# Optimization experiments

Hardware: AMD Instinct MI355X
Metric: run time of the kernel (lower is better)

The kernel has to match this reference:

```python
import jax, jax.numpy as jnp
import numpy as np

B = 8192       # batch (tokens)
D = 2048       # data_dim
DEPTH = 3      # tree depth: 1 root + 2 mid + 4 leaf experts
INIT = 0.02


def setup_inputs() -> dict:
    key = jax.random.key(0)
    ks = jax.random.split(key, 6)
    x = jax.random.normal(ks[0], (B, D), dtype=jnp.float32)
    # router output simulated as i.i.d. path bits (router is a frozen pretrained black box)
    path_mask = jax.random.randint(ks[1], (B, DEPTH), 0, 2, dtype=jnp.int32)
    W0 = jax.random.normal(ks[2], (D, D), dtype=jnp.float32) * INIT
    b0 = jnp.zeros((D,), dtype=jnp.float32)
    W1 = jax.random.normal(ks[3], (2, D, D), dtype=jnp.float32) * INIT  # depth-1 experts
    b1 = jnp.zeros((2, D), dtype=jnp.float32)
    W2 = jax.random.normal(ks[4], (4, D, D), dtype=jnp.float32) * INIT  # depth-2 (leaf) experts
    b2 = jnp.zeros((4, D), dtype=jnp.float32)
    return {"x": x, "W0": W0, "b0": b0, "W1": W1, "b1": b1,
            "W2": W2, "b2": b2, "path_mask": path_mask}


def reference(x, W0, b0, W1, b1, W2, b2, path_mask):
    # Root expert (depth 0): applied to all tokens.
    h0 = jax.nn.relu(x @ W0 + b0)                                  # [B, D]
    bit0 = path_mask[:, 0]                                          # routes depth-1 children
    bit1 = path_mask[:, 1]                                          # routes depth-2 children
    # Depth-1: 2 experts; dense compute then per-token select (static-shape MoE dispatch).
    h1_all = jax.nn.relu(jnp.einsum('bd,edf->bef', h0, W1) + b1)    # [B, 2, D]
    h1 = jnp.take_along_axis(h1_all, bit0[:, None, None].astype(jnp.int32), axis=1)[:, 0]
    # Depth-2 (leaves): 4 experts indexed by the 2-bit path.
    leaf = 2 * bit0 + bit1                                          # [B] in {0,1,2,3}
    h2_all = jax.nn.relu(jnp.einsum('bd,edf->bef', h1, W2) + b2)    # [B, 4, D]
    y = jnp.take_along_axis(h2_all, leaf[:, None, None].astype(jnp.int32), axis=1)[:, 0]
    return y
```

## Files before the change

kernel.cpp:

```cpp
#include <hip/hip_runtime.h>

#define BB 8192
#define DD 2048
#define NSLOT 7
#define NP1 (BB + 2*128)
#define NP2 (BB + 4*128)

typedef unsigned short u16;
typedef unsigned int   u32;
typedef unsigned long long u64;

typedef __bf16 bf16x8 __attribute__((ext_vector_type(8)));
typedef float  f32x4  __attribute__((ext_vector_type(4)));
typedef u16    u16x8  __attribute__((ext_vector_type(8)));

#define OFF_WT   0ull
#define OFF_XB   (OFF_WT + (size_t)NSLOT*DD*DD*2)
#define OFF_H0   (OFF_XB + (size_t)BB*DD*2)
#define OFF_P1   (OFF_H0 + (size_t)BB*DD*2)
#define OFF_P2   (OFF_P1 + (size_t)NP1*4)
#define OFF_META (OFF_P2 + (size_t)NP2*4)

__device__ __forceinline__ u16 f2bf(float f) {
  u32 u = __float_as_uint(f);
  u32 r = (u + 0x7FFFu + ((u >> 16) & 1u)) >> 16;
  return (u16)r;
}
__device__ __forceinline__ float bf2f(u16 u) {
  return __uint_as_float(((u32)u) << 16);
}

__device__ __forceinline__ void gld16(const void* g, void* l) {
  __builtin_amdgcn_global_load_lds(
      (const __attribute__((address_space(1))) void*)g,
      (__attribute__((address_space(3))) void*)l, 16, 0, 0);
}


__global__ void k_detect(const u16* x, int* meta) {
  __shared__ int cnt, cntz;
  if (threadIdx.x == 0) { cnt = 0; cntz = 0; }
  __syncthreads();
  u16 u = x[threadIdx.x * 17];
  int ex = (u >> 7) & 0xFF;
  int sane = (ex == 0) || (ex >= 112 && ex <= 143);
  atomicAdd(&cnt, sane);
  atomicAdd(&cntz, (u == 0) ? 1 : 0);
  __syncthreads();
  if (threadIdx.x == 0) meta[20] = (cnt >= 205 && cntz < 64) ? 1 : 0;
}

__global__ __launch_bounds__(1024) void k_route(const int* __restrict__ pm,
                                                int* __restrict__ p1,
                                                int* __restrict__ p2,
                                                int* __restrict__ meta) {
  __shared__ int cnt[6];
  __shared__ int cur[6];
  __shared__ int base1[2], base2[4];
  const int tid = threadIdx.x;
  const int lane = tid & 63;
  if (tid < 6) { cnt[tid] = 0; cur[tid] = 0; }
  __syncthreads();

  for (int i = tid; i < NP1; i += 1024) p1[i] = -1;
  for (int i = tid; i < NP2; i += 1024) p2[i] = -1;

  int myb0[8], myleaf[8];
  #pragma unroll
  for (int i = 0; i < 8; ++i) {
    int b = i * 1024 + tid;
    int b0 = pm[b*3] & 1, b1 = pm[b*3+1] & 1;
    myb0[i] = b0; myleaf[i] = b0*2 + b1;
  }
  #pragma unroll
  for (int i = 0; i < 8; ++i) {
    u64 m0 = __ballot(myb0[i] == 0);
    if (lane == 0) {
      atomicAdd(&cnt[0], __popcll(m0));
      atomicAdd(&cnt[1], 64 - __popcll(m0));
    }
    #pragma unroll
    for (int e = 0; e < 4; ++e) {
      u64 me = __ballot(myleaf[i] == e);
      if (lane == 0) atomicAdd(&cnt[2+e], __popcll(me));
    }
  }
  __syncthreads();
  if (tid == 0) {
    base1[0] = 0;
    base1[1] = (cnt[0] + 127) & ~127;
    meta[12] = 0; meta[13] = base1[1];
    meta[14] = base1[1] + ((cnt[1] + 127) & ~127);
    int b = 0;
    #pragma unroll
    for (int e = 0; e < 4; ++e) {
      base2[e] = b; meta[15+e] = b;
      b += (cnt[2+e] + 127) & ~127;
    }
    meta[19] = b;
  }
  __syncthreads();
  #pragma unroll
  for (int i = 0; i < 8; ++i) {
    int b = i * 1024 + tid;
    u64 lt = (1ull << lane) - 1ull;
    #pragma unroll
    for (int g = 0; g < 2; ++g) {
      u64 m = __ballot(myb0[i] == g);
      int pos = __popcll(m & lt);
      int wbase = 0;
      if (lane == 0 && m) wbase = atomicAdd(&cur[g], __popcll(m));
      wbase = __shfl(wbase, 0);
      if (myb0[i] == g) p1[base1[g] + wbase + pos] = b;
    }
    #pragma unroll
    for (int g = 0; g < 4; ++g) {
      u64 m = __ballot(myleaf[i] == g);
      int pos = __popcll(m & lt);
      int wbase = 0;
      if (lane == 0 && m) wbase = atomicAdd(&cur[2+g], __popcll(m));
      wbase = __shfl(wbase, 0);
      if (myleaf[i] == g) p2[base2[g] + wbase + pos] = b;
    }
  }
}

__global__ void k_cvtx(const void* __restrict__ x, u16* __restrict__ xb,
                       const int* __restrict__ meta) {
  int i = blockIdx.x * 256 + threadIdx.x;
  if (meta[20]) {
    ((uint4*)xb)[i] = ((const uint4*)x)[i];
  } else {
    const float4* p = (const float4*)x + (size_t)i * 2;
    float4 a = p[0], b = p[1];
    uint4 o;
    o.x = f2bf(a.x) | ((u32)f2bf(a.y) << 16);
    o.y = f2bf(a.z) | ((u32)f2bf(a.w) << 16);
    o.z = f2bf(b.x) | ((u32)f2bf(b.y) << 16);
    o.w = f2bf(b.z) | ((u32)f2bf(b.w) << 16);
    ((uint4*)xb)[i] = o;
  }
}

__global__ void k_wt(const void* __restrict__ W0, const void* __restrict__ W1,
                     const void* __restrict__ W2, u16* __restrict__ wt,
                     const int* __restrict__ meta) {
  __shared__ u16 tile[64][66];
  int bid = blockIdx.x;
  int slot = bid >> 10;
  int t = bid & 1023;
  int tr = t >> 5, tc = t & 31;
  const void* src; size_t eoff;
  if (slot == 0)      { src = W0; eoff = 0; }
  else if (slot <= 2) { src = W1; eoff = (size_t)(slot-1)*DD*DD; }
  else                { src = W2; eoff = (size_t)(slot-3)*DD*DD; }
  int r0 = tr*64, c0 = tc*64;
  int tid = threadIdx.x;
  int isbf = meta[20];
  #pragma unroll
  for (int i = 0; i < 4; ++i) {
    int idx = tid + i*256;
    int r = idx >> 4, c4 = (idx & 15) * 4;
    size_t goff = eoff + (size_t)(r0 + r)*DD + c0 + c4;
    u16 v0, v1, v2, v3;
    if (isbf) {
      ushort4 v = *(const ushort4*)((const u16*)src + goff);
      v0 = v.x; v1 = v.y; v2 = v.z; v3 = v.w;
    } else {
      float4 v = *(const float4*)((const float*)src + goff);
      v0 = f2bf(v.x); v1 = f2bf(v.y); v2 = f2bf(v.z); v3 = f2bf(v.w);
    }
    tile[r][c4+0] = v0; tile[r][c4+1] = v1;
    tile[r][c4+2] = v2; tile[r][c4+3] = v3;
  }
  __syncthreads();
  u16* dst = wt + (size_t)slot*DD*DD;
  #pragma unroll
  for (int i = 0; i < 2; ++i) {
    int idx = tid + i*256;
    int n = idx >> 3, j = idx & 7;
    u16x8 o;
    #pragma unroll
    for (int k = 0; k < 8; ++k) o[k] = tile[j*8 + k][n];
    *(u16x8*)&dst[(size_t)(c0 + n)*DD + r0 + j*8] = o;
  }
}

__global__ __launch_bounds__(256, 2) void k_gemm(
    const u16* __restrict__ A, const u16* __restrict__ Wt,
    const void* __restrict__ bias, const int* __restrict__ perm,
    const int* __restrict__ bases, int nexp,
    void* __restrict__ Out, int final_out, const int* __restrict__ meta) {
  __shared__ __align__(16) u16 As[128*32];
  __shared__ __align__(16) u16 Bs[128*32];

  const int tid  = threadIdx.x;
  const int wid  = tid >> 6;
  const int lane = tid & 63;
  const int m0 = blockIdx.y * 128;
  const int n0 = blockIdx.x * 128;

  int e = 0;
  if (nexp == 2)      e = (m0 >= bases[1]);
  else if (nexp == 4) e = (m0 >= bases[1]) + (m0 >= bases[2]) + (m0 >= bases[3]);
  const u16* W = Wt + (size_t)e * DD * DD;

  const u16* gA[2]; const u16* gB[2];
  u16* lA[2]; u16* lB[2];
  #pragma unroll
  for (int p = 0; p < 2; ++p) {
    int seg   = p*4 + wid;
    int boff  = seg*1024 + lane*16;
    int row   = boff >> 6;
    int chunk = (boff >> 4) & 3;
    int kk    = (chunk ^ ((row >> 1) & 3)) * 8;
    int gr = m0 + row;
    if (perm) { int t = perm[gr]; gr = (t < 0) ? 0 : t; }
    gA[p] = A + (size_t)gr * DD + kk;
    gB[p] = W + (size_t)(n0 + row) * DD + kk;
    lA[p] = (u16*)((char*)As + seg*1024);
    lB[p] = (u16*)((char*)Bs + seg*1024);
  }

  f32x4 zero = {0.0f, 0.0f, 0.0f, 0.0f};
  f32x4 acc[4][4];
  #pragma unroll
  for (int i = 0; i < 4; ++i)
    #pragma unroll
    for (int j = 0; j < 4; ++j) acc[i][j] = zero;

  const int wm = wid & 1, wn = wid >> 1;
  const int q = lane >> 4, cl = lane & 15;
  const int sw = q ^ ((cl >> 1) & 3);
  const int aoff  = (wm*64 + cl) * 32 + sw*8;
  const int boff2 = (wn*64 + cl) * 32 + sw*8;

  for (int k0 = 0; k0 < DD; k0 += 32) {
    gld16(gA[0] + k0, lA[0]);
    gld16(gA[1] + k0, lA[1]);
    gld16(gB[0] + k0, lB[0]);
    gld16(gB[1] + k0, lB[1]);
    __syncthreads();
    bf16x8 af[4], bf[4];
    #pragma unroll
    for (int mt = 0; mt < 4; ++mt) af[mt] = *(const bf16x8*)&As[aoff + mt*16*32];
    #pragma unroll
    for (int nt = 0; nt < 4; ++nt) bf[nt] = *(const bf16x8*)&Bs[boff2 + nt*16*32];
    #pragma unroll
    for (int mt = 0; mt < 4; ++mt)
      #pragma unroll
      for (int nt = 0; nt < 4; ++nt)
        acc[mt][nt] = __builtin_amdgcn_mfma_f32_16x16x32_bf16(af[mt], bf[nt], acc[mt][nt], 0, 0, 0);
    __syncthreads();
  }

  const int isbf = meta[20];
  float bv[4];
  #pragma unroll
  for (int nt = 0; nt < 4; ++nt) {
    int col = n0 + wn*64 + nt*16 + cl;
    bv[nt] = isbf ? bf2f(((const u16*)bias)[e*DD + col])
                  : ((const float*)bias)[e*DD + col];
  }
  #pragma unroll
  for (int mt = 0; mt < 4; ++mt) {
    int rbase = m0 + wm*64 + mt*16 + q*4;
    #pragma unroll
    for (int r = 0; r < 4; ++r) {
      int row = rbase + r;
      int orow = row;
      if (perm) { orow = perm[row]; if (orow < 0) continue; }
      #pragma unroll
      for (int nt = 0; nt < 4; ++nt) {
        int col = n0 + wn*64 + nt*16 + cl;
        float v = acc[mt][nt][r] + bv[nt];
        v = v > 0.0f ? v : 0.0f;
        if (!final_out || isbf) ((u16*)Out)[(size_t)orow*DD + col] = f2bf(v);
        else                    ((float*)Out)[(size_t)orow*DD + col] = v;
      }
    }
  }
}

extern "C" void kernel_launch(void* const* d_in, const int* in_sizes, int n_in,
                              void* d_out, int out_size, void* d_ws, size_t ws_size,
                              hipStream_t stream) {
  (void)in_sizes; (void)n_in; (void)out_size; (void)ws_size;
  const void* x  = d_in[0];
  const void* W0 = d_in[1];
  const void* b0 = d_in[2];
  const void* W1 = d_in[3];
  const void* b1 = d_in[4];
  const void* W2 = d_in[5];
  const void* b2 = d_in[6];
  const int*  pm = (const int*)d_in[7];

  char* ws  = (char*)d_ws;
  u16*  wt  = (u16*)(ws + OFF_WT);
  u16*  xb  = (u16*)(ws + OFF_XB);
  u16*  h0  = (u16*)(ws + OFF_H0);
  u16*  h1  = xb;
  int*  p1  = (int*)(ws + OFF_P1);
  int*  p2  = (int*)(ws + OFF_P2);
  int*  meta= (int*)(ws + OFF_META);

  hipLaunchKernelGGL(k_detect, dim3(1),  dim3(256),  0, stream, (const u16*)x, meta);
  hipLaunchKernelGGL(k_route,  dim3(1),  dim3(1024), 0, stream, pm, p1, p2, meta);
  hipLaunchKernelGGL(k_cvtx,   dim3(BB*DD/8/256), dim3(256), 0, stream, x, xb, meta);
  hipLaunchKernelGGL(k_wt,     dim3(7*1024), dim3(256), 0, stream, W0, W1, W2, wt, meta);

  hipLaunchKernelGGL(k_gemm, dim3(16, 64), dim3(256), 0, stream,
                     xb, wt, b0, (const int*)nullptr, (const int*)nullptr, 1,
                     (void*)h0, 0, meta);
  hipLaunchKernelGGL(k_gemm, dim3(16, 66), dim3(256), 0, stream,
                     h0, wt + (size_t)1*DD*DD, b1, p1, meta + 12, 2,
                     (void*)h1, 0, meta);
  hipLaunchKernelGGL(k_gemm, dim3(16, 68), dim3(256), 0, stream,
                     h1, wt + (size_t)3*DD*DD, b2, p2, meta + 15, 4,
                     d_out, 1, meta);
}
```

Measured before the change: 540.8 us.

## Fuse setup kernels into one launch and double-buffer GEMM LDS tiles

Merges the dtype-detect, routing, x conversion and weight transpose kernels into a single k_setup launch. Each block now recomputes the bf16 detection with a wavefront ballot instead of reading it from a prior kernel, which removes three launches and their serialization. The GEMM main loop moves to a two-buffer LDS scheme: the next K-slice is prefetched while MFMAs run on the current one, with one barrier per iteration instead of two. This doubles the GEMM's LDS use and relies on every block reaching the same detection result independently.

```diff
diff --git a/kernel.cpp b/kernel.cpp
--- a/kernel.cpp
+++ b/kernel.cpp
@@ -36,153 +36,147 @@
       (__attribute__((address_space(3))) void*)l, 16, 0, 0);
 }
 
-
-__global__ void k_detect(const u16* x, int* meta) {
-  __shared__ int cnt, cntz;
-  if (threadIdx.x == 0) { cnt = 0; cntz = 0; }
-  __syncthreads();
-  u16 u = x[threadIdx.x * 17];
+__device__ __forceinline__ int detect_bf(const u16* x) {
+  int lane = threadIdx.x & 63;
+  u16 u = x[lane * 33];
   int ex = (u >> 7) & 0xFF;
   int sane = (ex == 0) || (ex >= 112 && ex <= 143);
-  atomicAdd(&cnt, sane);
-  atomicAdd(&cntz, (u == 0) ? 1 : 0);
-  __syncthreads();
-  if (threadIdx.x == 0) meta[20] = (cnt >= 205 && cntz < 64) ? 1 : 0;
-}
-
-__global__ __launch_bounds__(1024) void k_route(const int* __restrict__ pm,
-                                                int* __restrict__ p1,
-                                                int* __restrict__ p2,
-                                                int* __restrict__ meta) {
-  __shared__ int cnt[6];
-  __shared__ int cur[6];
-  __shared__ int base1[2], base2[4];
+  u64 ms = __ballot(sane != 0);
+  u64 mz = __ballot(u == 0);
+  return (__popcll(ms) >= 52) && (__popcll(mz) < 16);
+}
+
+__global__ __launch_bounds__(256) void k_setup(
+    const void* __restrict__ xv, const void* __restrict__ W0,
+    const void* __restrict__ W1, const void* __restrict__ W2,
+    const int* __restrict__ pm, u16* __restrict__ xb, u16* __restrict__ wt,
+    int* __restrict__ p1, int* __restrict__ p2, int* __restrict__ meta) {
+  const int bid = blockIdx.x;
   const int tid = threadIdx.x;
-  const int lane = tid & 63;
-  if (tid < 6) { cnt[tid] = 0; cur[tid] = 0; }
-  __syncthreads();
-
-  for (int i = tid; i < NP1; i += 1024) p1[i] = -1;
-  for (int i = tid; i < NP2; i += 1024) p2[i] = -1;
-
-  int myb0[8], myleaf[8];
-  #pragma unroll
-  for (int i = 0; i < 8; ++i) {
-    int b = i * 1024 + tid;
-    int b0 = pm[b*3] & 1, b1 = pm[b*3+1] & 1;
-    myb0[i] = b0; myleaf[i] = b0*2 + b1;
-  }
-  #pragma unroll
-  for (int i = 0; i < 8; ++i) {
-    u64 m0 = __ballot(myb0[i] == 0);
-    if (lane == 0) {
-      atomicAdd(&cnt[0], __popcll(m0));
-      atomicAdd(&cnt[1], 64 - __popcll(m0));
-    }
-    #pragma unroll
-    for (int e = 0; e < 4; ++e) {
-      u64 me = __ballot(myleaf[i] == e);
-      if (lane == 0) atomicAdd(&cnt[2+e], __popcll(me));
-    }
-  }
-  __syncthreads();
-  if (tid == 0) {
-    base1[0] = 0;
-    base1[1] = (cnt[0] + 127) & ~127;
-    meta[12] = 0; meta[13] = base1[1];
-    meta[14] = base1[1] + ((cnt[1] + 127) & ~127);
-    int b = 0;
-    #pragma unroll
-    for (int e = 0; e < 4; ++e) {
-      base2[e] = b; meta[15+e] = b;
-      b += (cnt[2+e] + 127) & ~127;
-    }
-    meta[19] = b;
-  }
-  __syncthreads();
-  #pragma unroll
-  for (int i = 0; i < 8; ++i) {
-    int b = i * 1024 + tid;
-    u64 lt = (1ull << lane) - 1ull;
-    #pragma unroll
-    for (int g = 0; g < 2; ++g) {
-      u64 m = __ballot(myb0[i] == g);
-      int pos = __popcll(m & lt);
-      int wbase = 0;
-      if (lane == 0 && m) wbase = atomicAdd(&cur[g], __popcll(m));
-      wbase = __shfl(wbase, 0);
-      if (myb0[i] == g) p1[base1[g] + wbase + pos] = b;
-    }
-    #pragma unroll
-    for (int g = 0; g < 4; ++g) {
-      u64 m = __ballot(myleaf[i] == g);
-      int pos = __popcll(m & lt);
-      int wbase = 0;
-      if (lane == 0 && m) wbase = atomicAdd(&cur[2+g], __popcll(m));
-      wbase = __shfl(wbase, 0);
-      if (myleaf[i] == g) p2[base2[g] + wbase + pos] = b;
-    }
-  }
-}
-
-__global__ void k_cvtx(const void* __restrict__ x, u16* __restrict__ xb,
-                       const int* __restrict__ meta) {
-  int i = blockIdx.x * 256 + threadIdx.x;
-  if (meta[20]) {
-    ((uint4*)xb)[i] = ((const uint4*)x)[i];
-  } else {
-    const float4* p = (const float4*)x + (size_t)i * 2;
-    float4 a = p[0], b = p[1];
-    uint4 o;
-    o.x = f2bf(a.x) | ((u32)f2bf(a.y) << 16);
-    o.y = f2bf(a.z) | ((u32)f2bf(a.w) << 16);
-    o.z = f2bf(b.x) | ((u32)f2bf(b.y) << 16);
-    o.w = f2bf(b.z) | ((u32)f2bf(b.w) << 16);
-    ((uint4*)xb)[i] = o;
-  }
-}
-
-__global__ void k_wt(const void* __restrict__ W0, const void* __restrict__ W1,
-                     const void* __restrict__ W2, u16* __restrict__ wt,
-                     const int* __restrict__ meta) {
-  __shared__ u16 tile[64][66];
-  int bid = blockIdx.x;
-  int slot = bid >> 10;
-  int t = bid & 1023;
-  int tr = t >> 5, tc = t & 31;
-  const void* src; size_t eoff;
-  if (slot == 0)      { src = W0; eoff = 0; }
-  else if (slot <= 2) { src = W1; eoff = (size_t)(slot-1)*DD*DD; }
-  else                { src = W2; eoff = (size_t)(slot-3)*DD*DD; }
-  int r0 = tr*64, c0 = tc*64;
-  int tid = threadIdx.x;
-  int isbf = meta[20];
-  #pragma unroll
-  for (int i = 0; i < 4; ++i) {
-    int idx = tid + i*256;
-    int r = idx >> 4, c4 = (idx & 15) * 4;
-    size_t goff = eoff + (size_t)(r0 + r)*DD + c0 + c4;
-    u16 v0, v1, v2, v3;
+  const u16* x = (const u16*)xv;
+
+  if (bid == 0) {
+    int isbf = detect_bf(x);
+    if (tid == 0) meta[20] = isbf;
+    __shared__ int cnt[6], cur[6], base1[2], base2[4];
+    const int lane = tid & 63;
+    if (tid < 6) { cnt[tid] = 0; cur[tid] = 0; }
+    __syncthreads();
+    for (int i = tid; i < NP1; i += 256) p1[i] = -1;
+    for (int i = tid; i < NP2; i += 256) p2[i] = -1;
+    for (int c = 0; c < 32; ++c) {
+      int b = c * 256 + tid;
+      int b0 = pm[b*3] & 1, b1v = pm[b*3+1] & 1;
+      int leaf = b0*2 + b1v;
+      u64 m0 = __ballot(b0 == 0);
+      if (lane == 0) {
+        atomicAdd(&cnt[0], __popcll(m0));
+        atomicAdd(&cnt[1], 64 - __popcll(m0));
+      }
+      #pragma unroll
+      for (int e = 0; e < 4; ++e) {
+        u64 me = __ballot(leaf == e);
+        if (lane == 0) atomicAdd(&cnt[2+e], __popcll(me));
+      }
+    }
+    __syncthreads();
+    if (tid == 0) {
+      base1[0] = 0;
+      base1[1] = (cnt[0] + 127) & ~127;
+      meta[12] = 0; meta[13] = base1[1];
+      meta[14] = base1[1] + ((cnt[1] + 127) & ~127);
+      int b = 0;
+      #pragma unroll
+      for (int e = 0; e < 4; ++e) {
+        base2[e] = b; meta[15+e] = b;
+        b += (cnt[2+e] + 127) & ~127;
+      }
+    }
+    __syncthreads();
+    for (int c = 0; c < 32; ++c) {
+      int b = c * 256 + tid;
+      int b0 = pm[b*3] & 1, b1v = pm[b*3+1] & 1;
+      int leaf = b0*2 + b1v;
+      u64 lt = (1ull << lane) - 1ull;
+      #pragma unroll
+      for (int g = 0; g < 2; ++g) {
+        u64 m = __ballot(b0 == g);
+        int pos = __popcll(m & lt);
+        int wbase = 0;
+        if (lane == 0 && m) wbase = atomicAdd(&cur[g], __popcll(m));
+        wbase = __shfl(wbase, 0);
+        if (b0 == g) p1[base1[g] + wbase + pos] = b;
+      }
+      #pragma unroll
+      for (int g = 0; g < 4; ++g) {
+        u64 m = __ballot(leaf == g);
+        int pos = __popcll(m & lt);
+        int wbase = 0;
+        if (lane == 0 && m) wbase = atomicAdd(&cur[2+g], __popcll(m));
+        wbase = __shfl(wbase, 0);
+        if (leaf == g) p2[base2[g] + wbase + pos] = b;
+      }
+    }
+    return;
+  }
+
+  if (bid <= 8192) {
+    int isbf = detect_bf(x);
+    int i = (bid - 1) * 256 + tid;
     if (isbf) {
-      ushort4 v = *(const ushort4*)((const u16*)src + goff);
-      v0 = v.x; v1 = v.y; v2 = v.z; v3 = v.w;
+      ((uint4*)xb)[i] = ((const uint4*)xv)[i];
     } else {
-      float4 v = *(const float4*)((const float*)src + goff);
-      v0 = f2bf(v.x); v1 = f2bf(v.y); v2 = f2bf(v.z); v3 = f2bf(v.w);
-    }
-    tile[r][c4+0] = v0; tile[r][c4+1] = v1;
-    tile[r][c4+2] = v2; tile[r][c4+3] = v3;
-  }
-  __syncthreads();
-  u16* dst = wt + (size_t)slot*DD*DD;
-  #pragma unroll
-  for (int i = 0; i < 2; ++i) {
-    int idx = tid + i*256;
-    int n = idx >> 3, j = idx & 7;
-    u16x8 o;
-    #pragma unroll
-    for (int k = 0; k < 8; ++k) o[k] = tile[j*8 + k][n];
-    *(u16x8*)&dst[(size_t)(c0 + n)*DD + r0 + j*8] = o;
+      const float4* p = (const float4*)xv + (size_t)i * 2;
+      float4 a = p[0], b = p[1];
+      uint4 o;
+      o.x = f2bf(a.x) | ((u32)f2bf(a.y) << 16);
+      o.y = f2bf(a.z) | ((u32)f2bf(a.w) << 16);
+      o.z = f2bf(b.x) | ((u32)f2bf(b.y) << 16);
+      o.w = f2bf(b.z) | ((u32)f2bf(b.w) << 16);
+      ((uint4*)xb)[i] = o;
+    }
+    return;
+  }
+
+  {
+    int isbf = detect_bf(x);
+    __shared__ u16 tile[64][66];
+    int wb = bid - 8193;
+    int slot = wb >> 10;
+    int t = wb & 1023;
+    int tr = t >> 5, tc = t & 31;
+    const void* src; size_t eoff;
+    if (slot == 0)      { src = W0; eoff = 0; }
+    else if (slot <= 2) { src = W1; eoff = (size_t)(slot-1)*DD*DD; }
+    else                { src = W2; eoff = (size_t)(slot-3)*DD*DD; }
+    int r0 = tr*64, c0 = tc*64;
+    #pragma unroll
+    for (int i = 0; i < 4; ++i) {
+      int idx = tid + i*256;
+      int r = idx >> 4, c4 = (idx & 15) * 4;
+      size_t goff = eoff + (size_t)(r0 + r)*DD + c0 + c4;
+      u16 v0, v1, v2, v3;
+      if (isbf) {
+        ushort4 v = *(const ushort4*)((const u16*)src + goff);
+        v0 = v.x; v1 = v.y; v2 = v.z; v3 = v.w;
+      } else {
+        float4 v = *(const float4*)((const float*)src + goff);
+        v0 = f2bf(v.x); v1 = f2bf(v.y); v2 = f2bf(v.z); v3 = f2bf(v.w);
+      }
+      tile[r][c4+0] = v0; tile[r][c4+1] = v1;
+      tile[r][c4+2] = v2; tile[r][c4+3] = v3;
+    }
+    __syncthreads();
+    u16* dst = wt + (size_t)slot*DD*DD;
+    #pragma unroll
+    for (int i = 0; i < 2; ++i) {
+      int idx = tid + i*256;
+      int n = idx >> 3, j = idx & 7;
+      u16x8 o;
+      #pragma unroll
+      for (int k = 0; k < 8; ++k) o[k] = tile[j*8 + k][n];
+      *(u16x8*)&dst[(size_t)(c0 + n)*DD + r0 + j*8] = o;
+    }
   }
 }
 
@@ -191,8 +185,8 @@
     const void* __restrict__ bias, const int* __restrict__ perm,
     const int* __restrict__ bases, int nexp,
     void* __restrict__ Out, int final_out, const int* __restrict__ meta) {
-  __shared__ __align__(16) u16 As[128*32];
-  __shared__ __align__(16) u16 Bs[128*32];
+  __shared__ __align__(16) u16 As[2][4096];
+  __shared__ __align__(16) u16 Bs[2][4096];
 
   const int tid  = threadIdx.x;
   const int wid  = tid >> 6;
@@ -206,7 +200,7 @@
   const u16* W = Wt + (size_t)e * DD * DD;
 
   const u16* gA[2]; const u16* gB[2];
-  u16* lA[2]; u16* lB[2];
+  int loff[2];
   #pragma unroll
   for (int p = 0; p < 2; ++p) {
     int seg   = p*4 + wid;
@@ -218,8 +212,7 @@
     if (perm) { int t = perm[gr]; gr = (t < 0) ? 0 : t; }
     gA[p] = A + (size_t)gr * DD + kk;
     gB[p] = W + (size_t)(n0 + row) * DD + kk;
-    lA[p] = (u16*)((char*)As + seg*1024);
-    lB[p] = (u16*)((char*)Bs + seg*1024);
+    loff[p] = seg * 512 + lane * 8;
   }
 
   f32x4 zero = {0.0f, 0.0f, 0.0f, 0.0f};
@@ -235,23 +228,33 @@
   const int aoff  = (wm*64 + cl) * 32 + sw*8;
   const int boff2 = (wn*64 + cl) * 32 + sw*8;
 
+  #pragma unroll
+  for (int p = 0; p < 2; ++p) {
+    gld16(gA[p], &As[0][loff[p]]);
+    gld16(gB[p], &Bs[0][loff[p]]);
+  }
+
   for (int k0 = 0; k0 < DD; k0 += 32) {
-    gld16(gA[0] + k0, lA[0]);
-    gld16(gA[1] + k0, lA[1]);
-    gld16(gB[0] + k0, lB[0]);
-    gld16(gB[1] + k0, lB[1]);
-    __syncthreads();
+    const int buf = (k0 >> 5) & 1;
+    __syncthreads();
+    if (k0 + 32 < DD) {
+      const int nb = buf ^ 1;
+      #pragma unroll
+      for (int p = 0; p < 2; ++p) {
+        gld16(gA[p] + k0 + 32, &As[nb][loff[p]]);
+        gld16(gB[p] + k0 + 32, &Bs[nb][loff[p]]);
+      }
+    }
     bf16x8 af[4], bf[4];
     #pragma unroll
-    for (int mt = 0; mt < 4; ++mt) af[mt] = *(const bf16x8*)&As[aoff + mt*16*32];
-    #pragma unroll
-    for (int nt = 0; nt < 4; ++nt) bf[nt] = *(const bf16x8*)&Bs[boff2 + nt*16*32];
+    for (int mt = 0; mt < 4; ++mt) af[mt] = *(const bf16x8*)&As[buf][aoff + mt*512];
+    #pragma unroll
+    for (int nt = 0; nt < 4; ++nt) bf[nt] = *(const bf16x8*)&Bs[buf][boff2 + nt*512];
     #pragma unroll
     for (int mt = 0; mt < 4; ++mt)
       #pragma unroll
       for (int nt = 0; nt < 4; ++nt)
         acc[mt][nt] = __builtin_amdgcn_mfma_f32_16x16x32_bf16(af[mt], bf[nt], acc[mt][nt], 0, 0, 0);
-    __syncthreads();
   }
 
   const int isbf = meta[20];
@@ -304,10 +307,8 @@
   int*  p2  = (int*)(ws + OFF_P2);
   int*  meta= (int*)(ws + OFF_META);
 
-  hipLaunchKernelGGL(k_detect, dim3(1),  dim3(256),  0, stream, (const u16*)x, meta);
-  hipLaunchKernelGGL(k_route,  dim3(1),  dim3(1024), 0, stream, pm, p1, p2, meta);
-  hipLaunchKernelGGL(k_cvtx,   dim3(BB*DD/8/256), dim3(256), 0, stream, x, xb, meta);
-  hipLaunchKernelGGL(k_wt,     dim3(7*1024), dim3(256), 0, stream, W0, W1, W2, wt, meta);
+  hipLaunchKernelGGL(k_setup, dim3(1 + 8192 + 7*1024), dim3(256), 0, stream,
+                     x, W0, W1, W2, pm, xb, wt, p1, p2, meta);
 
   hipLaunchKernelGGL(k_gemm, dim3(16, 64), dim3(256), 0, stream,
                      xb, wt, b0, (const int*)nullptr, (const int*)nullptr, 1,
```

Measured after the change: 564.0 us. 1.04x slower.
